# Kernel optimization log

Measured on AMD Instinct MI355X. Metric: run time of the kernel, lower is better.

Reference implementation:

```python
import jax, jax.numpy as jnp
import numpy as np

NUM_IR = 10
EPS = 1e-6
SQRT_IR = float(np.sqrt(NUM_IR))


def norm_activation(x, bias):
    # e3nn nn.NormActivation with tanh, normalize=True, bias=True, epsilon=1e-6
    # x: [..., mul, 3] (mul copies of l=1 irreps)
    norms = jnp.sqrt(jnp.sum(x * x, axis=-1) + EPS * EPS)  # [..., mul]
    scal = jnp.tanh(norms + bias) / norms                   # act(norm+b)/norm
    return x * scal[..., None]


def setup_inputs() -> dict:
    key = jax.random.key(0)
    ks = jax.random.split(key, 10)
    B, P = 4096, 256
    s = 0.5
    return {
        "vectors_1b": jax.random.normal(ks[0], (B, 3), jnp.float32),
        "invar_2b": jax.random.normal(ks[1], (B, P, 2), jnp.float32),
        "vectors_2b": jax.random.normal(ks[2], (B, P, 6), jnp.float32),
        # scalar MLP (torch.nn.Linear 2->10, 10->10)
        "W1": jax.random.normal(ks[3], (2, NUM_IR), jnp.float32) * s,
        "b1": jnp.zeros((NUM_IR,), jnp.float32),
        "W2": jax.random.normal(ks[4], (NUM_IR, NUM_IR), jnp.float32) * s,
        "b2": jnp.zeros((NUM_IR,), jnp.float32),
        # o3.Linear weights (equivariant channel mixing of 1o irreps)
        "lw1": jax.random.normal(ks[5], (1, NUM_IR), jnp.float32),   # 1x1o -> 10x1o
        "nb1": jnp.zeros((NUM_IR,), jnp.float32),                    # NormActivation bias
        "lw2": jax.random.normal(ks[6], (NUM_IR, NUM_IR), jnp.float32),  # 10x1o -> 10x1o
        "nb2": jnp.zeros((NUM_IR,), jnp.float32),
        "wf": jax.random.normal(ks[7], (NUM_IR,), jnp.float32),      # 10x1o -> 1x1o
    }


def reference(vectors_1b, invar_2b, vectors_2b, W1, b1, W2, b2, lw1, nb1, lw2, nb2, wf):
    B, P, _ = vectors_2b.shape
    # scalar branch: MLP on invariant pair features -> [B, P, 10] (10x0e)
    y = jax.nn.relu(invar_2b @ W1 + b1)
    y = jax.nn.relu(y @ W2 + b2)
    # equivariant branch: take components 3:6 as 1x1o vector
    v = vectors_2b[..., 3:6]                                   # [B, P, 3]
    # o3.Linear 1x1o -> 10x1o (fan_in = 1, path norm 1/sqrt(1))
    x = v[..., None, :] * lw1[0][:, None]                      # [B, P, 10, 3]
    x = norm_activation(x, nb1)
    # o3.Linear 10x1o -> 10x1o (path norm 1/sqrt(10))
    x = jnp.einsum("bpui,uv->bpvi", x, lw2) / SQRT_IR
    x = norm_activation(x, nb2)
    # ElementwiseTensorProduct(10x0e, 10x1o): per-channel scalar*vector
    x = y[..., None] * x                                       # [B, P, 10, 3]
    # final o3.Linear 10x1o -> 1x1o (path norm 1/sqrt(10))
    x = jnp.einsum("bpui,u->bpi", x, wf) / SQRT_IR             # [B, P, 3]
    t = jnp.sum(x, axis=1)                                     # [B, 3]
    return jnp.cross(vectors_1b, t)
```

## Files before the change

### kernel.cpp

```cpp
#include <hip/hip_runtime.h>


#define P_PTS 256
constexpr float EPS2 = 1e-12f;
constexpr float INV_SQRT10 = 0.31622776601683794f;

__device__ __forceinline__ float fast_tanh(float x) {
    float ax = fminf(fabsf(x), 40.0f);
    float e  = __expf(2.0f * ax);
    float t  = fmaf(-2.0f, __builtin_amdgcn_rcpf(e + 1.0f), 1.0f);
    return copysignf(t, x);
}

__global__ __launch_bounds__(256) void trq_kernel(
    const float* __restrict__ v1b,
    const float* __restrict__ invar,
    const float* __restrict__ v2b,
    const float* __restrict__ W1,
    const float* __restrict__ b1,
    const float* __restrict__ W2,
    const float* __restrict__ b2,
    const float* __restrict__ lw1,
    const float* __restrict__ nb1,
    const float* __restrict__ lw2,
    const float* __restrict__ nb2,
    const float* __restrict__ wf,
    float* __restrict__ out)
{
    __shared__ float sW1[20], sb1[10], sW2[100], sb2[10];
    __shared__ float slw1[10], snb1[10], slw2[100], snb2[10], swf[10];
    __shared__ float red[4][3];

    const int t = threadIdx.x;
    if (t < 20)  sW1[t] = W1[t];
    if (t < 100) { sW2[t] = W2[t]; slw2[t] = lw2[t]; }
    if (t < 10) {
        sb1[t] = b1[t];  sb2[t] = b2[t];  slw1[t] = lw1[t];
        snb1[t] = nb1[t]; snb2[t] = nb2[t]; swf[t] = wf[t];
    }
    __syncthreads();

    const int b = blockIdx.x;
    const size_t bp = (size_t)b * P_PTS + t;

    const float i0 = invar[bp * 2 + 0];
    const float i1 = invar[bp * 2 + 1];
    const float* vp = v2b + bp * 6;
    const float v0 = vp[3], v1 = vp[4], v2 = vp[5];
    const float vv = fmaf(v0, v0, fmaf(v1, v1, v2 * v2));

    float y1[10];
    #pragma unroll
    for (int u = 0; u < 10; ++u)
        y1[u] = fmaxf(fmaf(i0, sW1[u], fmaf(i1, sW1[10 + u], sb1[u])), 0.f);

    float y2[10];
    #pragma unroll
    for (int vi = 0; vi < 10; ++vi) {
        float acc = sb2[vi];
        #pragma unroll
        for (int u = 0; u < 10; ++u) acc = fmaf(y1[u], sW2[u * 10 + vi], acc);
        y2[vi] = fmaxf(acc, 0.f);
    }

    float a[10];
    #pragma unroll
    for (int u = 0; u < 10; ++u) {
        float l = slw1[u];
        float q = fmaf(l * l, vv, EPS2);
        float r = __builtin_amdgcn_rsqf(q);
        float n = q * r;
        a[u] = l * fast_tanh(n + snb1[u]) * r;
    }

    float s = 0.f;
    #pragma unroll
    for (int vi = 0; vi < 10; ++vi) {
        float c = 0.f;
        #pragma unroll
        for (int u = 0; u < 10; ++u) c = fmaf(a[u], slw2[u * 10 + vi], c);
        c *= INV_SQRT10;
        float q = fmaf(c * c, vv, EPS2);
        float r = __builtin_amdgcn_rsqf(q);
        float n = q * r;
        float d = c * fast_tanh(n + snb2[vi]) * r;
        s = fmaf(y2[vi] * d, swf[vi], s);
    }
    s *= INV_SQRT10;

    float px = s * v0, py = s * v1, pz = s * v2;

    #pragma unroll
    for (int off = 32; off > 0; off >>= 1) {
        px += __shfl_down(px, off);
        py += __shfl_down(py, off);
        pz += __shfl_down(pz, off);
    }
    const int wid = t >> 6;
    if ((t & 63) == 0) { red[wid][0] = px; red[wid][1] = py; red[wid][2] = pz; }
    __syncthreads();

    if (t == 0) {
        float tx = red[0][0] + red[1][0] + red[2][0] + red[3][0];
        float ty = red[0][1] + red[1][1] + red[2][1] + red[3][1];
        float tz = red[0][2] + red[1][2] + red[2][2] + red[3][2];
        float a0 = v1b[b * 3 + 0], a1 = v1b[b * 3 + 1], a2 = v1b[b * 3 + 2];
        out[b * 3 + 0] = fmaf(a1, tz, -a2 * ty);
        out[b * 3 + 1] = fmaf(a2, tx, -a0 * tz);
        out[b * 3 + 2] = fmaf(a0, ty, -a1 * tx);
    }
}

extern "C" void kernel_launch(void* const* d_in, const int* in_sizes, int n_in,
                              void* d_out, int out_size, void* d_ws, size_t ws_size,
                              hipStream_t stream) {
    const float* v1b   = (const float*)d_in[0];
    const float* invar = (const float*)d_in[1];
    const float* v2b   = (const float*)d_in[2];
    const float* W1    = (const float*)d_in[3];
    const float* b1    = (const float*)d_in[4];
    const float* W2    = (const float*)d_in[5];
    const float* b2    = (const float*)d_in[6];
    const float* lw1   = (const float*)d_in[7];
    const float* nb1   = (const float*)d_in[8];
    const float* lw2   = (const float*)d_in[9];
    const float* nb2   = (const float*)d_in[10];
    const float* wf    = (const float*)d_in[11];
    float* out = (float*)d_out;

    const int B = in_sizes[0] / 3;
    trq_kernel<<<B, P_PTS, 0, stream>>>(v1b, invar, v2b, W1, b1, W2, b2,
                                        lw1, nb1, lw2, nb2, wf, out);
}
```

Measured before the change: 110.9 us.

## Drop LDS weight staging, fold scale constants, simplify tanh and vectorize loads

```diff
diff --git a/kernel.cpp b/kernel.cpp
--- a/kernel.cpp
+++ b/kernel.cpp
@@ -3,13 +3,10 @@
 
 #define P_PTS 256
 constexpr float EPS2 = 1e-12f;
-constexpr float INV_SQRT10 = 0.31622776601683794f;
 
-__device__ __forceinline__ float fast_tanh(float x) {
-    float ax = fminf(fabsf(x), 40.0f);
-    float e  = __expf(2.0f * ax);
-    float t  = fmaf(-2.0f, __builtin_amdgcn_rcpf(e + 1.0f), 1.0f);
-    return copysignf(t, x);
+__device__ __forceinline__ float tanh_f(float x) {
+    float e = __expf(2.0f * x);
+    return fmaf(-2.0f, __builtin_amdgcn_rcpf(e + 1.0f), 1.0f);
 }
 
 __global__ __launch_bounds__(256) void trq_kernel(
@@ -27,50 +24,42 @@
     const float* __restrict__ wf,
     float* __restrict__ out)
 {
-    __shared__ float sW1[20], sb1[10], sW2[100], sb2[10];
-    __shared__ float slw1[10], snb1[10], slw2[100], snb2[10], swf[10];
     __shared__ float red[4][3];
 
     const int t = threadIdx.x;
-    if (t < 20)  sW1[t] = W1[t];
-    if (t < 100) { sW2[t] = W2[t]; slw2[t] = lw2[t]; }
-    if (t < 10) {
-        sb1[t] = b1[t];  sb2[t] = b2[t];  slw1[t] = lw1[t];
-        snb1[t] = nb1[t]; snb2[t] = nb2[t]; swf[t] = wf[t];
-    }
-    __syncthreads();
-
     const int b = blockIdx.x;
     const size_t bp = (size_t)b * P_PTS + t;
 
-    const float i0 = invar[bp * 2 + 0];
-    const float i1 = invar[bp * 2 + 1];
+    const float2 iv = *(const float2*)(invar + bp * 2);
     const float* vp = v2b + bp * 6;
-    const float v0 = vp[3], v1 = vp[4], v2 = vp[5];
-    const float vv = fmaf(v0, v0, fmaf(v1, v1, v2 * v2));
+    const float v0 = vp[3];
+    const float2 v12 = *(const float2*)(vp + 4);
+    const float v1 = v12.x, v2 = v12.y;
+    const float vv   = fmaf(v0, v0, fmaf(v1, v1, v2 * v2));
+    const float vv10 = vv * 0.1f;
 
     float y1[10];
     #pragma unroll
     for (int u = 0; u < 10; ++u)
-        y1[u] = fmaxf(fmaf(i0, sW1[u], fmaf(i1, sW1[10 + u], sb1[u])), 0.f);
+        y1[u] = fmaxf(fmaf(iv.x, W1[u], fmaf(iv.y, W1[10 + u], b1[u])), 0.f);
 
-    float y2[10];
+    float zw[10];
     #pragma unroll
     for (int vi = 0; vi < 10; ++vi) {
-        float acc = sb2[vi];
+        float acc = b2[vi];
         #pragma unroll
-        for (int u = 0; u < 10; ++u) acc = fmaf(y1[u], sW2[u * 10 + vi], acc);
-        y2[vi] = fmaxf(acc, 0.f);
+        for (int u = 0; u < 10; ++u) acc = fmaf(y1[u], W2[u * 10 + vi], acc);
+        zw[vi] = fmaxf(acc, 0.f) * (wf[vi] * 0.1f);
     }
 
     float a[10];
     #pragma unroll
     for (int u = 0; u < 10; ++u) {
-        float l = slw1[u];
+        float l = lw1[u];
         float q = fmaf(l * l, vv, EPS2);
         float r = __builtin_amdgcn_rsqf(q);
         float n = q * r;
-        a[u] = l * fast_tanh(n + snb1[u]) * r;
+        a[u] = (l * tanh_f(n + nb1[u])) * r;
     }
 
     float s = 0.f;
@@ -78,15 +67,12 @@
     for (int vi = 0; vi < 10; ++vi) {
         float c = 0.f;
         #pragma unroll
-        for (int u = 0; u < 10; ++u) c = fmaf(a[u], slw2[u * 10 + vi], c);
-        c *= INV_SQRT10;
-        float q = fmaf(c * c, vv, EPS2);
+        for (int u = 0; u < 10; ++u) c = fmaf(a[u], lw2[u * 10 + vi], c);
+        float q = fmaf(c * c, vv10, EPS2);
         float r = __builtin_amdgcn_rsqf(q);
         float n = q * r;
-        float d = c * fast_tanh(n + snb2[vi]) * r;
-        s = fmaf(y2[vi] * d, swf[vi], s);
+        s = fmaf(zw[vi] * c, tanh_f(n + nb2[vi]) * r, s);
     }
-    s *= INV_SQRT10;
 
     float px = s * v0, py = s * v1, pz = s * v2;
 
```

New measurement: 108.5 us. 1.02x faster.
